# Performance work log

Measured on AMD Instinct MI355X. Metric: run time of the kernel, lower is better.

The kernel has to match this reference:

```python
import jax, jax.numpy as jnp
import numpy as np

DIM = 512
NUM_HEADS = 8
HEAD_DIM = DIM // NUM_HEADS
GAMMA = 1.0


def setup_inputs() -> dict:
    key = jax.random.key(0)
    ks = jax.random.split(key, 10)
    B, S = 2, 2048
    x_real = jax.random.normal(ks[0], (B, S, DIM), dtype=jnp.float32)
    x_imag = jax.random.normal(ks[1], (B, S, DIM), dtype=jnp.float32)
    def xavier(k, fan_in, fan_out):
        lim = float(np.sqrt(6.0 / (fan_in + fan_out)))
        return jax.random.uniform(k, (fan_in, fan_out), jnp.float32, -lim, lim)
    # torch Linear(in,out): weight [out,in]; we store transposed [in,out]
    Wq = xavier(ks[2], 2 * DIM, DIM); bq = jnp.zeros((DIM,), jnp.float32)
    Wk = xavier(ks[3], 2 * DIM, DIM); bk = jnp.zeros((DIM,), jnp.float32)
    Wv = xavier(ks[4], 2 * DIM, DIM); bv = jnp.zeros((DIM,), jnp.float32)
    Wo = xavier(ks[5], DIM, 2 * DIM); bo = jnp.zeros((2 * DIM,), jnp.float32)
    return {"x_real": x_real, "x_imag": x_imag, "Wq": Wq, "bq": bq,
            "Wk": Wk, "bk": bk, "Wv": Wv, "bv": bv, "Wo": Wo, "bo": bo}


def reference(x_real, x_imag, Wq, bq, Wk, bk, Wv, bv, Wo, bo):
    B, S, _ = x_real.shape
    real_embed = jnp.concatenate([x_real, x_imag], axis=-1)  # [B,S,2*dim]
    def proj(W, b):
        y = real_embed @ W + b                               # [B,S,dim]
        return y.reshape(B, S, NUM_HEADS, HEAD_DIM).transpose(0, 2, 1, 3)  # [B,H,S,d]
    Q = proj(Wq, bq)
    K = proj(Wk, bk)
    V = proj(Wv, bv)
    # softmax over head_dim is broadcast-invariant, so the Bhattacharyya
    # coefficient sum_d sqrt(p_i[d]*q_j[d]) factorizes into a matmul.
    sp = jnp.sqrt(jax.nn.softmax(Q, axis=-1))  # [B,H,S,d]
    sq = jnp.sqrt(jax.nn.softmax(K, axis=-1))  # [B,H,S,d]
    bc = jnp.einsum('bhid,bhjd->bhij', sp, sq)  # Bhattacharyya coeff [B,H,S,S]
    bc = jnp.clip(bc, -1.0, 1.0)
    dist = jnp.arccos(bc)
    attn = jax.nn.softmax(-GAMMA * dist * dist, axis=-1)  # [B,H,S,S]
    attended = jnp.einsum('bhij,bhjd->bhid', attn, V)
    attended = attended.transpose(0, 2, 1, 3).reshape(B, S, DIM)
    out = attended @ Wo + bo  # [B,S,2*dim] = concat(real_out, imag_out)
    return out
```

## Files before the change

### kernel.cpp

```cpp
#include <hip/hip_runtime.h>
#include <math.h>


typedef __attribute__((ext_vector_type(8))) short short8;
typedef __attribute__((ext_vector_type(4))) short bf16x4;
typedef __attribute__((ext_vector_type(4))) float f32x4;
typedef __attribute__((ext_vector_type(2))) float f32x2;

#define MFMA(a, b, c) __builtin_amdgcn_mfma_f32_16x16x32_bf16((a), (b), (c), 0, 0, 0)

static __device__ __forceinline__ short f2bf(float f) {
    unsigned u = __float_as_uint(f);
    u += 0x7fffu + ((u >> 16) & 1u);
    return (short)(u >> 16);
}

static __device__ __forceinline__ void gld_lds16(const short* g, short* l) {
    __builtin_amdgcn_global_load_lds(
        (const __attribute__((address_space(1))) unsigned int*)g,
        (__attribute__((address_space(3))) unsigned int*)l, 16, 0, 0);
}

__global__ __launch_bounds__(256) void convert_x(
    const float* __restrict__ xr, const float* __restrict__ xi,
    short* __restrict__ xb)
{
    int idx = blockIdx.x * 256 + threadIdx.x;
    int e = idx << 2;
    int m = e >> 10, k = e & 1023;
    const float* src = (k < 512) ? xr : xi;
    float4 t = *(const float4*)(src + (size_t)m * 512 + (k & 511));
    unsigned lo = (unsigned short)f2bf(t.x) | ((unsigned)(unsigned short)f2bf(t.y) << 16);
    unsigned hi = (unsigned short)f2bf(t.z) | ((unsigned)(unsigned short)f2bf(t.w) << 16);
    uint2 o; o.x = lo; o.y = hi;
    *(uint2*)(xb + e) = o;
}

__global__ __launch_bounds__(256) void transpose_w(
    const float* __restrict__ Wq, const float* __restrict__ Wk,
    const float* __restrict__ Wv, const float* __restrict__ Wo,
    short* __restrict__ wqt, short* __restrict__ wkt,
    short* __restrict__ wvt, short* __restrict__ wot)
{
    __shared__ float t[32][33];
    const int z = blockIdx.z;
    const float* src = (z == 0) ? Wq : (z == 1) ? Wk : (z == 2) ? Wv : Wo;
    short* dst = (z == 0) ? wqt : (z == 1) ? wkt : (z == 2) ? wvt : wot;
    const int K = (z < 3) ? 1024 : 512;
    const int N = (z < 3) ? 512 : 1024;
    const int n0 = blockIdx.x << 5, k0 = blockIdx.y << 5;
    if (n0 >= N || k0 >= K) return;
    const int tx = threadIdx.x & 31, ty = threadIdx.x >> 5;
    #pragma unroll
    for (int i = 0; i < 4; ++i)
        t[ty + 8 * i][tx] = src[(size_t)(k0 + ty + 8 * i) * N + n0 + tx];
    __syncthreads();
    #pragma unroll
    for (int i = 0; i < 4; ++i)
        dst[(size_t)(n0 + ty + 8 * i) * K + k0 + tx] = f2bf(t[tx][ty + 8 * i]);
}

__global__ __launch_bounds__(64) void qkv_mfma(
    const short* __restrict__ xb, const short* __restrict__ wcat,
    const float* __restrict__ bq, const float* __restrict__ bk,
    const float* __restrict__ bv,
    short* __restrict__ sp, short* __restrict__ sq, short* __restrict__ vt)
{
    __shared__ short As[3][64 * 32];
    __shared__ short Bs[3][64 * 32];
    const int jb = blockIdx.x;
    const int m0 = blockIdx.y << 6;
    const int lane = threadIdx.x;
    const int l = lane & 15, quad = lane >> 4;

    const int srow = lane >> 2;
    const int sseg = (lane & 3) << 3;
    const short* gA = xb   + (size_t)(m0        + srow) * 1024 + sseg;
    const short* gB = wcat + (size_t)((jb << 6) + srow) * 1024 + sseg;

    auto STAGE = [&](int bb, int kk) {
        const int k0 = kk << 5;
        #pragma unroll
        for (int t = 0; t < 4; ++t) {
            gld_lds16(gA + k0 + t * 16 * 1024, &As[bb][t << 9]);
            gld_lds16(gB + k0 + t * 16 * 1024, &Bs[bb][t << 9]);
        }
    };

    STAGE(0, 0);
    STAGE(1, 1);
    asm volatile("s_waitcnt vmcnt(8)" ::: "memory");

    const f32x4 z4 = {0.f, 0.f, 0.f, 0.f};
    f32x4 acc[4][4];
    #pragma unroll
    for (int i = 0; i < 4; ++i)
        #pragma unroll
        for (int j = 0; j < 4; ++j) acc[i][j] = z4;

    int cb = 0, sb = 2;
    #pragma unroll 1
    for (int kt = 0; kt < 32; ++kt) {
        STAGE(sb, (kt + 2) & 31);
        const short* Al = &As[cb][0];
        const short* Bl = &Bs[cb][0];
        short8 af[4], bfr[4];
        #pragma unroll
        for (int i = 0; i < 4; ++i)
            af[i] = *(const short8*)(Al + (((i << 4) + l) << 5) + (quad << 3));
        #pragma unroll
        for (int j = 0; j < 4; ++j)
            bfr[j] = *(const short8*)(Bl + (((j << 4) + l) << 5) + (quad << 3));
        #pragma unroll
        for (int i = 0; i < 4; ++i)
            #pragma unroll
            for (int j = 0; j < 4; ++j)
                acc[i][j] = MFMA(af[i], bfr[j], acc[i][j]);
        asm volatile("s_waitcnt vmcnt(8)" ::: "memory");
        cb = (cb == 2) ? 0 : cb + 1;
        sb = (sb == 2) ? 0 : sb + 1;
    }

    const int op = jb >> 3;
    const int h  = jb & 7;

    if (op < 2) {
        short* dst = (op == 0) ? sp : sq;
        const float* bias = (op == 0) ? bq : bk;
        float bcol[4];
        #pragma unroll
        for (int nt = 0; nt < 4; ++nt) bcol[nt] = bias[(h << 6) + (nt << 4) + l];
        #pragma unroll
        for (int i = 0; i < 4; ++i) {
            #pragma unroll
            for (int reg = 0; reg < 4; ++reg) {
                const int r = m0 + (i << 4) + (quad << 2) + reg;
                const int b = r >> 11, s = r & 2047;
                float v[4];
                #pragma unroll
                for (int nt = 0; nt < 4; ++nt) v[nt] = acc[i][nt][reg] + bcol[nt];
                float mx = fmaxf(fmaxf(v[0], v[1]), fmaxf(v[2], v[3]));
                #pragma unroll
                for (int msk = 1; msk < 16; msk <<= 1) mx = fmaxf(mx, __shfl_xor(mx, msk));
                float e[4], ssum = 0.f;
                #pragma unroll
                for (int nt = 0; nt < 4; ++nt) { e[nt] = __expf(v[nt] - mx); ssum += e[nt]; }
                #pragma unroll
                for (int msk = 1; msk < 16; msk <<= 1) ssum += __shfl_xor(ssum, msk);
                float inv = 1.0f / ssum;
                short* o = dst + ((size_t)((b << 3) + h) * 2048 + s) * 64 + l;
                #pragma unroll
                for (int nt = 0; nt < 4; ++nt)
                    o[nt << 4] = f2bf(sqrtf(e[nt] * inv));
            }
        }
    } else {
        float bcol[4];
        #pragma unroll
        for (int nt = 0; nt < 4; ++nt) bcol[nt] = bv[(h << 6) + (nt << 4) + l];
        #pragma unroll
        for (int i = 0; i < 4; ++i) {
            const int sb2 = m0 + (i << 4) + (quad << 2);
            const int b = sb2 >> 11, s = sb2 & 2047;
            #pragma unroll
            for (int nt = 0; nt < 4; ++nt) {
                const int d = (nt << 4) + l;
                bf16x4 pk;
                #pragma unroll
                for (int reg = 0; reg < 4; ++reg)
                    pk[reg] = f2bf(acc[i][nt][reg] + bcol[nt]);
                *(bf16x4*)(vt + ((size_t)((b << 3) + h) * 64 + d) * 2048 + s) = pk;
            }
        }
    }
}

__global__ __launch_bounds__(256, 4) void attn_mfma(
    const short* __restrict__ sp, const short* __restrict__ sq,
    const short* __restrict__ vt, short* __restrict__ attB)
{
    __shared__ __align__(16) short sqT[2][64 * 64];
    __shared__ __align__(16) short vtT[2][64 * 64];
    __shared__ __align__(16) short Pb[4][16 * 64];
    __shared__ float denB[4][16];
    const int bh = blockIdx.y;
    const int m0 = blockIdx.x << 6;
    const int tid = threadIdx.x;
    const int w = tid >> 6, lane = tid & 63;
    const int l = lane & 15, quad = lane >> 4;
    const int l7 = l & 7;

    const short* spB = sp + (size_t)bh * 2048 * 64;
    const short* sqB = sq + (size_t)bh * 2048 * 64;
    const short* vtB = vt + (size_t)bh * 64 * 2048;

    const short* apr = spB + (size_t)(m0 + w * 16 + l) * 64 + quad * 8;
    short8 aq0 = *(const short8*)(apr);
    short8 aq1 = *(const short8*)(apr + 32);
    short8 nq0 = aq0 ^ (short)0x8000;
    short8 nq1 = aq1 ^ (short)0x8000;

    const int srow = tid >> 2;
    const int scol = (tid & 3) * 16;
    const short* sqG = sqB + (size_t)srow * 64 + scol;
    const short* vtG = vtB + (size_t)srow * 2048 + scol;
    const int sl0 = (tid & 3) << 1;
    const int sw0 = srow * 64 + (((sl0    ) ^ (srow & 7)) << 3);
    const int sw1 = srow * 64 + (((sl0 | 1) ^ (srow & 7)) << 3);

    const int sRd = (quad ^ l7) << 3;

    {
        short8 a0 = *(const short8*)(sqG);
        short8 a1 = *(const short8*)(sqG + 8);
        short8 b0 = *(const short8*)(vtG);
        short8 b1 = *(const short8*)(vtG + 8);
        *(short8*)(&sqT[0][sw0]) = a0;
        *(short8*)(&sqT[0][sw1]) = a1;
        *(short8*)(&vtT[0][sw0]) = b0;
        *(short8*)(&vtT[0][sw1]) = b1;
    }
    __syncthreads();

    const f32x4 z4 = {0.f, 0.f, 0.f, 0.f};
    const f32x4 ones4 = {1.f, 1.f, 1.f, 1.f};
    f32x4 acc[4] = {z4, z4, z4, z4};
    f32x2 den2 = {0.f, 0.f};
    short* Pw = &Pb[w][0];

    #pragma unroll 1
    for (int jt = 0; jt < 32; ++jt) {
        const int cb = jt & 1, nb = cb ^ 1;
        const int j0n = ((jt + 1) & 31) << 6;
        short8 na0 = *(const short8*)(sqG + (size_t)j0n * 64);
        short8 na1 = *(const short8*)(sqG + (size_t)j0n * 64 + 8);
        short8 nb0 = *(const short8*)(vtG + j0n);
        short8 nb1 = *(const short8*)(vtG + j0n + 8);

        const short* sqL = &sqT[cb][0];
        #pragma unroll
        for (int nt = 0; nt < 4; ++nt) {
            const short* ar = sqL + ((nt * 16 + l) << 6);
            short8 sa0 = *(const short8*)(ar + sRd);
            short8 sa1 = *(const short8*)(ar + (sRd ^ 32));
            f32x4 p = MFMA(sa0, nq0, ones4);
            p = MFMA(sa1, nq1, p);
            f32x2 u01 = {p[0], p[1]};
            f32x2 u23 = {p[2], p[3]};
            const f32x2 zz = {0.f, 0.f};
#if __has_builtin(__builtin_elementwise_max)
            u01 = __builtin_elementwise_max(u01, zz);
            u23 = __builtin_elementwise_max(u23, zz);
#else
            u01.x = fmaxf(u01.x, 0.f); u01.y = fmaxf(u01.y, 0.f);
            u23.x = fmaxf(u23.x, 0.f); u23.y = fmaxf(u23.y, 0.f);
#endif
            f32x2 t01 = {0.000922f, 0.000922f};
            f32x2 t23 = t01;
            t01 = t01 * u01 + 0.00152228f;  t23 = t23 * u23 + 0.00152228f;
            t01 = t01 * u01 + 0.00384801f;  t23 = t23 * u23 + 0.00384801f;
            t01 = t01 * u01 + 0.01015873f;  t23 = t23 * u23 + 0.01015873f;
            t01 = t01 * u01 + 0.02857143f;  t23 = t23 * u23 + 0.02857143f;
            t01 = t01 * u01 + 0.08888889f;  t23 = t23 * u23 + 0.08888889f;
            t01 = t01 * u01 + 0.33333333f;  t23 = t23 * u23 + 0.33333333f;
            t01 = t01 * u01 + 2.0f;         t23 = t23 * u23 + 2.0f;
            f32x2 w01 = u01 * t01;
            f32x2 w23 = u23 * t23;
            float e0 = __expf(-w01.x), e1 = __expf(-w01.y);
            float e2 = __expf(-w23.x), e3 = __expf(-w23.y);
            f32x2 es = {e0 + e2, e1 + e3};
            den2 += es;
            uint2 pk;
            pk.x = (__float_as_uint(e0) >> 16) | (__float_as_uint(e1) & 0xffff0000u);
            pk.y = (__float_as_uint(e2) >> 16) | (__float_as_uint(e3) & 0xffff0000u);
            *(uint2*)(&Pw[(l << 6) + ((((nt << 1) + (quad >> 1)) ^ l7) << 3)
                          + ((quad & 1) << 2)]) = pk;
        }

        const short* pr = Pw + (l << 6);
        short8 pa0 = *(const short8*)(pr + sRd);
        short8 pa1 = *(const short8*)(pr + (sRd ^ 32));
        const short* vL = &vtT[cb][0];
        #pragma unroll
        for (int t4 = 0; t4 < 4; ++t4) {
            const short* vr = vL + ((t4 * 16 + l) << 6);
            short8 vb0 = *(const short8*)(vr + sRd);
            short8 vb1 = *(const short8*)(vr + (sRd ^ 32));
            acc[t4] = MFMA(pa0, vb0, acc[t4]);
            acc[t4] = MFMA(pa1, vb1, acc[t4]);
        }

        *(short8*)(&sqT[nb][sw0]) = na0;
        *(short8*)(&sqT[nb][sw1]) = na1;
        *(short8*)(&vtT[nb][sw0]) = nb0;
        *(short8*)(&vtT[nb][sw1]) = nb1;
        __syncthreads();
    }

    float den = den2.x + den2.y;
    den += __shfl_xor(den, 16);
    den += __shfl_xor(den, 32);
    if (lane < 16) denB[w][l] = den;
    float invd[4];
    #pragma unroll
    for (int reg = 0; reg < 4; ++reg)
        invd[reg] = 1.0f / denB[w][quad * 4 + reg];

    const int b = bh >> 3, hh = bh & 7;
    #pragma unroll
    for (int t4 = 0; t4 < 4; ++t4)
        #pragma unroll
        for (int reg = 0; reg < 4; ++reg) {
            const int row = m0 + w * 16 + quad * 4 + reg;
            attB[((size_t)(b * 2048 + row)) * 512 + hh * 64 + t4 * 16 + l] =
                f2bf(acc[t4][reg] * invd[reg]);
        }
}

__global__ __launch_bounds__(64) void out_mfma(
    const short* __restrict__ attB, const short* __restrict__ wot,
    const float* __restrict__ bo, float* __restrict__ out)
{
    __shared__ short As[3][64 * 32];
    __shared__ short Bs[3][64 * 32];
    const int n0 = blockIdx.x << 6;
    const int m0 = blockIdx.y << 6;
    const int lane = threadIdx.x;
    const int l = lane & 15, quad = lane >> 4;

    const int srow = lane >> 2;
    const int sseg = (lane & 3) << 3;
    const short* gA = attB + (size_t)(m0 + srow) * 512 + sseg;
    const short* gB = wot  + (size_t)(n0 + srow) * 512 + sseg;

    auto STAGE = [&](int bb, int kk) {
        const int k0 = kk << 5;
        #pragma unroll
        for (int t = 0; t < 4; ++t) {
            gld_lds16(gA + k0 + t * 16 * 512, &As[bb][t << 9]);
            gld_lds16(gB + k0 + t * 16 * 512, &Bs[bb][t << 9]);
        }
    };

    STAGE(0, 0);
    STAGE(1, 1);
    asm volatile("s_waitcnt vmcnt(8)" ::: "memory");

    const f32x4 z4 = {0.f, 0.f, 0.f, 0.f};
    f32x4 acc[4][4];
    #pragma unroll
    for (int i = 0; i < 4; ++i)
        #pragma unroll
        for (int j = 0; j < 4; ++j) acc[i][j] = z4;

    int cb = 0, sb = 2;
    #pragma unroll 1
    for (int kt = 0; kt < 16; ++kt) {
        STAGE(sb, (kt + 2) & 15);
        const short* Al = &As[cb][0];
        const short* Bl = &Bs[cb][0];
        short8 af[4], bfr[4];
        #pragma unroll
        for (int i = 0; i < 4; ++i)
            af[i] = *(const short8*)(Al + (((i << 4) + l) << 5) + (quad << 3));
        #pragma unroll
        for (int j = 0; j < 4; ++j)
            bfr[j] = *(const short8*)(Bl + (((j << 4) + l) << 5) + (quad << 3));
        #pragma unroll
        for (int i = 0; i < 4; ++i)
            #pragma unroll
            for (int j = 0; j < 4; ++j)
                acc[i][j] = MFMA(af[i], bfr[j], acc[i][j]);
        asm volatile("s_waitcnt vmcnt(8)" ::: "memory");
        cb = (cb == 2) ? 0 : cb + 1;
        sb = (sb == 2) ? 0 : sb + 1;
    }

    float bcol[4];
    #pragma unroll
    for (int nt = 0; nt < 4; ++nt) bcol[nt] = bo[n0 + (nt << 4) + l];
    #pragma unroll
    for (int i = 0; i < 4; ++i)
        #pragma unroll
        for (int reg = 0; reg < 4; ++reg) {
            const int m = m0 + (i << 4) + (quad << 2) + reg;
            float* o = out + (size_t)m * 1024 + n0 + l;
            #pragma unroll
            for (int nt = 0; nt < 4; ++nt)
                o[nt << 4] = acc[i][nt][reg] + bcol[nt];
        }
}

extern "C" void kernel_launch(void* const* d_in, const int* in_sizes, int n_in,
                              void* d_out, int out_size, void* d_ws, size_t ws_size,
                              hipStream_t stream) {
    const float* xr = (const float*)d_in[0];
    const float* xi = (const float*)d_in[1];
    const float* Wq = (const float*)d_in[2];
    const float* bq = (const float*)d_in[3];
    const float* Wk = (const float*)d_in[4];
    const float* bk = (const float*)d_in[5];
    const float* Wv = (const float*)d_in[6];
    const float* bv = (const float*)d_in[7];
    const float* Wo = (const float*)d_in[8];
    const float* bo = (const float*)d_in[9];
    float* out = (float*)d_out;

    short* base = (short*)d_ws;
    short* xb   = base;
    short* wqt  = xb  + 4194304;
    short* wkt  = wqt + 524288;
    short* wvt  = wkt + 524288;
    short* wot  = wvt + 524288;
    short* spW  = wot + 524288;
    short* sqW  = spW + 2097152;
    short* vtW  = sqW + 2097152;
    short* attB = vtW + 2097152;

    hipLaunchKernelGGL(convert_x, dim3(4096), dim3(256), 0, stream, xr, xi, xb);
    hipLaunchKernelGGL(transpose_w, dim3(32, 32, 4), dim3(256), 0, stream,
                       Wq, Wk, Wv, Wo, wqt, wkt, wvt, wot);
    hipLaunchKernelGGL(qkv_mfma, dim3(24, 64), dim3(64), 0, stream,
                       xb, wqt, bq, bk, bv, spW, sqW, vtW);
    hipLaunchKernelGGL(attn_mfma, dim3(32, 16), dim3(256), 0, stream,
                       spW, sqW, vtW, attB);
    hipLaunchKernelGGL(out_mfma, dim3(16, 64), dim3(64), 0, stream,
                       attB, wot, bo, out);
}
```

Measured before the change: 184.6 us.

## Split attention over key halves, keep P in registers, use exp2 polynomial

```diff
diff --git a/kernel.cpp b/kernel.cpp
--- a/kernel.cpp
+++ b/kernel.cpp
@@ -6,6 +6,7 @@
 typedef __attribute__((ext_vector_type(4))) short bf16x4;
 typedef __attribute__((ext_vector_type(4))) float f32x4;
 typedef __attribute__((ext_vector_type(2))) float f32x2;
+typedef __attribute__((ext_vector_type(4))) unsigned int u32x4;
 
 #define MFMA(a, b, c) __builtin_amdgcn_mfma_f32_16x16x32_bf16((a), (b), (c), 0, 0, 0)
 
@@ -177,14 +178,14 @@
 
 __global__ __launch_bounds__(256, 4) void attn_mfma(
     const short* __restrict__ sp, const short* __restrict__ sq,
-    const short* __restrict__ vt, short* __restrict__ attB)
+    const short* __restrict__ vt,
+    float* __restrict__ pnum, float* __restrict__ pden)
 {
     __shared__ __align__(16) short sqT[2][64 * 64];
     __shared__ __align__(16) short vtT[2][64 * 64];
-    __shared__ __align__(16) short Pb[4][16 * 64];
-    __shared__ float denB[4][16];
     const int bh = blockIdx.y;
     const int m0 = blockIdx.x << 6;
+    const int z  = blockIdx.z;
     const int tid = threadIdx.x;
     const int w = tid >> 6, lane = tid & 63;
     const int l = lane & 15, quad = lane >> 4;
@@ -195,48 +196,57 @@
     const short* vtB = vt + (size_t)bh * 64 * 2048;
 
     const short* apr = spB + (size_t)(m0 + w * 16 + l) * 64 + quad * 8;
-    short8 aq0 = *(const short8*)(apr);
-    short8 aq1 = *(const short8*)(apr + 32);
-    short8 nq0 = aq0 ^ (short)0x8000;
-    short8 nq1 = aq1 ^ (short)0x8000;
+    short8 nq0 = (*(const short8*)(apr)) ^ (short)0x8000;
+    short8 nq1 = (*(const short8*)(apr + 32)) ^ (short)0x8000;
 
     const int srow = tid >> 2;
-    const int scol = (tid & 3) * 16;
+    const int t3 = tid & 3;
+    const int scol = t3 * 16;
     const short* sqG = sqB + (size_t)srow * 64 + scol;
     const short* vtG = vtB + (size_t)srow * 2048 + scol;
-    const int sl0 = (tid & 3) << 1;
+    const int sl0 = t3 << 1;
     const int sw0 = srow * 64 + (((sl0    ) ^ (srow & 7)) << 3);
     const int sw1 = srow * 64 + (((sl0 | 1) ^ (srow & 7)) << 3);
+    int vwo[4];
+    #pragma unroll
+    for (int m = 0; m < 4; ++m)
+        vwo[m] = srow * 64 + ((((t3 >> 1) * 4 + m) ^ (srow & 7)) << 3)
+               + ((t3 & 1) << 2);
 
     const int sRd = (quad ^ l7) << 3;
 
     {
-        short8 a0 = *(const short8*)(sqG);
-        short8 a1 = *(const short8*)(sqG + 8);
-        short8 b0 = *(const short8*)(vtG);
-        short8 b1 = *(const short8*)(vtG + 8);
+        const int j0 = (z << 4) << 6;
+        short8 a0 = *(const short8*)(sqG + (size_t)j0 * 64);
+        short8 a1 = *(const short8*)(sqG + (size_t)j0 * 64 + 8);
+        short8 b0 = *(const short8*)(vtG + j0);
+        short8 b1 = *(const short8*)(vtG + j0 + 8);
         *(short8*)(&sqT[0][sw0]) = a0;
         *(short8*)(&sqT[0][sw1]) = a1;
-        *(short8*)(&vtT[0][sw0]) = b0;
-        *(short8*)(&vtT[0][sw1]) = b1;
+        u32x4 u0 = __builtin_bit_cast(u32x4, b0);
+        u32x4 u1 = __builtin_bit_cast(u32x4, b1);
+        *(uint2*)(&vtT[0][vwo[0]]) = (uint2){u0.x, u0.y};
+        *(uint2*)(&vtT[0][vwo[1]]) = (uint2){u0.z, u0.w};
+        *(uint2*)(&vtT[0][vwo[2]]) = (uint2){u1.x, u1.y};
+        *(uint2*)(&vtT[0][vwo[3]]) = (uint2){u1.z, u1.w};
     }
     __syncthreads();
 
+    const f32x4 ones4 = {1.f, 1.f, 1.f, 1.f};
     const f32x4 z4 = {0.f, 0.f, 0.f, 0.f};
-    const f32x4 ones4 = {1.f, 1.f, 1.f, 1.f};
     f32x4 acc[4] = {z4, z4, z4, z4};
     f32x2 den2 = {0.f, 0.f};
-    short* Pw = &Pb[w][0];
 
     #pragma unroll 1
-    for (int jt = 0; jt < 32; ++jt) {
-        const int cb = jt & 1, nb = cb ^ 1;
-        const int j0n = ((jt + 1) & 31) << 6;
+    for (int jtl = 0; jtl < 16; ++jtl) {
+        const int cb = jtl & 1, nb = cb ^ 1;
+        const int j0n = ((z << 4) + ((jtl + 1) & 15)) << 6;
         short8 na0 = *(const short8*)(sqG + (size_t)j0n * 64);
         short8 na1 = *(const short8*)(sqG + (size_t)j0n * 64 + 8);
         short8 nb0 = *(const short8*)(vtG + j0n);
         short8 nb1 = *(const short8*)(vtG + j0n + 8);
 
+        uint2 pk[4];
         const short* sqL = &sqT[cb][0];
         #pragma unroll
         for (int nt = 0; nt < 4; ++nt) {
@@ -255,31 +265,36 @@
             u01.x = fmaxf(u01.x, 0.f); u01.y = fmaxf(u01.y, 0.f);
             u23.x = fmaxf(u23.x, 0.f); u23.y = fmaxf(u23.y, 0.f);
 #endif
-            f32x2 t01 = {0.000922f, 0.000922f};
+            f32x2 t01 = {-0.00133017f, -0.00133017f};
             f32x2 t23 = t01;
-            t01 = t01 * u01 + 0.00152228f;  t23 = t23 * u23 + 0.00152228f;
-            t01 = t01 * u01 + 0.00384801f;  t23 = t23 * u23 + 0.00384801f;
-            t01 = t01 * u01 + 0.01015873f;  t23 = t23 * u23 + 0.01015873f;
-            t01 = t01 * u01 + 0.02857143f;  t23 = t23 * u23 + 0.02857143f;
-            t01 = t01 * u01 + 0.08888889f;  t23 = t23 * u23 + 0.08888889f;
-            t01 = t01 * u01 + 0.33333333f;  t23 = t23 * u23 + 0.33333333f;
-            t01 = t01 * u01 + 2.0f;         t23 = t23 * u23 + 2.0f;
+            t01 = t01 * u01 - 0.00219618f;  t23 = t23 * u23 - 0.00219618f;
+            t01 = t01 * u01 - 0.00555151f;  t23 = t23 * u23 - 0.00555151f;
+            t01 = t01 * u01 - 0.01465597f;  t23 = t23 * u23 - 0.01465597f;
+            t01 = t01 * u01 - 0.04121986f;  t23 = t23 * u23 - 0.04121986f;
+            t01 = t01 * u01 - 0.12823956f;  t23 = t23 * u23 - 0.12823956f;
+            t01 = t01 * u01 - 0.48089834f;  t23 = t23 * u23 - 0.48089834f;
+            t01 = t01 * u01 - 2.88539008f;  t23 = t23 * u23 - 2.88539008f;
             f32x2 w01 = u01 * t01;
             f32x2 w23 = u23 * t23;
-            float e0 = __expf(-w01.x), e1 = __expf(-w01.y);
-            float e2 = __expf(-w23.x), e3 = __expf(-w23.y);
+#if __has_builtin(__builtin_amdgcn_exp2f)
+            float e0 = __builtin_amdgcn_exp2f(w01.x);
+            float e1 = __builtin_amdgcn_exp2f(w01.y);
+            float e2 = __builtin_amdgcn_exp2f(w23.x);
+            float e3 = __builtin_amdgcn_exp2f(w23.y);
+#else
+            float e0 = exp2f(w01.x), e1 = exp2f(w01.y);
+            float e2 = exp2f(w23.x), e3 = exp2f(w23.y);
+#endif
             f32x2 es = {e0 + e2, e1 + e3};
             den2 += es;
-            uint2 pk;
-            pk.x = (__float_as_uint(e0) >> 16) | (__float_as_uint(e1) & 0xffff0000u);
-            pk.y = (__float_as_uint(e2) >> 16) | (__float_as_uint(e3) & 0xffff0000u);
-            *(uint2*)(&Pw[(l << 6) + ((((nt << 1) + (quad >> 1)) ^ l7) << 3)
-                          + ((quad & 1) << 2)]) = pk;
-        }
-
-        const short* pr = Pw + (l << 6);
-        short8 pa0 = *(const short8*)(pr + sRd);
-        short8 pa1 = *(const short8*)(pr + (sRd ^ 32));
+            pk[nt].x = (__float_as_uint(e0) >> 16) | (__float_as_uint(e1) & 0xffff0000u);
+            pk[nt].y = (__float_as_uint(e2) >> 16) | (__float_as_uint(e3) & 0xffff0000u);
+        }
+
+        u32x4 c0; c0.x = pk[0].x; c0.y = pk[0].y; c0.z = pk[1].x; c0.w = pk[1].y;
+        u32x4 c1; c1.x = pk[2].x; c1.y = pk[2].y; c1.z = pk[3].x; c1.w = pk[3].y;
+        short8 pa0 = __builtin_bit_cast(short8, c0);
+        short8 pa1 = __builtin_bit_cast(short8, c1);
         const short* vL = &vtT[cb][0];
         #pragma unroll
         for (int t4 = 0; t4 < 4; ++t4) {
@@ -292,29 +307,61 @@
 
         *(short8*)(&sqT[nb][sw0]) = na0;
         *(short8*)(&sqT[nb][sw1]) = na1;
-        *(short8*)(&vtT[nb][sw0]) = nb0;
-        *(short8*)(&vtT[nb][sw1]) = nb1;
+        u32x4 u0 = __builtin_bit_cast(u32x4, nb0);
+        u32x4 u1 = __builtin_bit_cast(u32x4, nb1);
+        *(uint2*)(&vtT[nb][vwo[0]]) = (uint2){u0.x, u0.y};
+        *(uint2*)(&vtT[nb][vwo[1]]) = (uint2){u0.z, u0.w};
+        *(uint2*)(&vtT[nb][vwo[2]]) = (uint2){u1.x, u1.y};
+        *(uint2*)(&vtT[nb][vwo[3]]) = (uint2){u1.z, u1.w};
         __syncthreads();
     }
 
     float den = den2.x + den2.y;
     den += __shfl_xor(den, 16);
     den += __shfl_xor(den, 32);
-    if (lane < 16) denB[w][l] = den;
-    float invd[4];
-    #pragma unroll
-    for (int reg = 0; reg < 4; ++reg)
-        invd[reg] = 1.0f / denB[w][quad * 4 + reg];
+    if (lane < 16)
+        pden[(size_t)z * 32768 + bh * 2048 + m0 + w * 16 + l] = den;
 
     const int b = bh >> 3, hh = bh & 7;
+    float* np = pnum + (size_t)z * 4096 * 512;
     #pragma unroll
     for (int t4 = 0; t4 < 4; ++t4)
         #pragma unroll
         for (int reg = 0; reg < 4; ++reg) {
             const int row = m0 + w * 16 + quad * 4 + reg;
-            attB[((size_t)(b * 2048 + row)) * 512 + hh * 64 + t4 * 16 + l] =
-                f2bf(acc[t4][reg] * invd[reg]);
-        }
+            np[((size_t)(b * 2048 + row)) * 512 + hh * 64 + t4 * 16 + l] =
+                acc[t4][reg];
+        }
+}
+
+__global__ __launch_bounds__(256) void combine_attn(
+    const float* __restrict__ pnum, const float* __restrict__ pden,
+    short* __restrict__ attB)
+{
+    const int idx = (blockIdx.x * 256 + threadIdx.x) << 3;
+    const int r = idx >> 9;
+    const int c = idx & 511;
+    const int hh = c >> 6;
+    const int bh = ((r >> 11) << 3) + hh;
+    const int srow = r & 2047;
+    const float d = pden[bh * 2048 + srow] + pden[32768 + bh * 2048 + srow];
+    const float inv = 1.0f / d;
+    const float* n0 = pnum + (size_t)r * 512 + c;
+    const float* n1 = n0 + (size_t)4096 * 512;
+    float4 a0 = *(const float4*)(n0);
+    float4 a1 = *(const float4*)(n0 + 4);
+    float4 b0 = *(const float4*)(n1);
+    float4 b1 = *(const float4*)(n1 + 4);
+    short8 o;
+    o[0] = f2bf((a0.x + b0.x) * inv);
+    o[1] = f2bf((a0.y + b0.y) * inv);
+    o[2] = f2bf((a0.z + b0.z) * inv);
+    o[3] = f2bf((a0.w + b0.w) * inv);
+    o[4] = f2bf((a1.x + b1.x) * inv);
+    o[5] = f2bf((a1.y + b1.y) * inv);
+    o[6] = f2bf((a1.z + b1.z) * inv);
+    o[7] = f2bf((a1.w + b1.w) * inv);
+    *(short8*)(attB + idx) = o;
 }
 
 __global__ __launch_bounds__(64) void out_mfma(
@@ -416,14 +463,18 @@
     short* sqW  = spW + 2097152;
     short* vtW  = sqW + 2097152;
     short* attB = vtW + 2097152;
+    float* pnum = (float*)(attB + 2097152);
+    float* pden = pnum + 8388608;
 
     hipLaunchKernelGGL(convert_x, dim3(4096), dim3(256), 0, stream, xr, xi, xb);
     hipLaunchKernelGGL(transpose_w, dim3(32, 32, 4), dim3(256), 0, stream,
                        Wq, Wk, Wv, Wo, wqt, wkt, wvt, wot);
     hipLaunchKernelGGL(qkv_mfma, dim3(24, 64), dim3(64), 0, stream,
                        xb, wqt, bq, bk, bv, spW, sqW, vtW);
-    hipLaunchKernelGGL(attn_mfma, dim3(32, 16), dim3(256), 0, stream,
-                       spW, sqW, vtW, attB);
+    hipLaunchKernelGGL(attn_mfma, dim3(32, 16, 2), dim3(256), 0, stream,
+                       spW, sqW, vtW, pnum, pden);
+    hipLaunchKernelGGL(combine_attn, dim3(1024), dim3(256), 0, stream,
+                       pnum, pden, attB);
     hipLaunchKernelGGL(out_mfma, dim3(16, 64), dim3(64), 0, stream,
                        attB, wot, bo, out);
 }
```

New measurement: 180.2 us. -2.4%, faster.
